# Performance work log

Hardware: AMD Instinct MI355X
Metric: run time of the kernel (lower is better)

The kernel has to match this reference:

```python
import jax, jax.numpy as jnp
import numpy as np

EPS = 1e-5  # InstanceNorm2d default eps


def setup_inputs() -> dict:
    key = jax.random.key(0)
    k1, k2, k3, k4, k5, k6 = jax.random.split(key, 6)
    B, N, C, KV, H = 8, 4096, 512, 960, 4
    dq, dk = C // 4, KV // 4
    emb1 = jax.random.normal(k1, (B, N, C), dtype=jnp.float32)
    emb_all = jax.random.normal(k2, (B, N, KV), dtype=jnp.float32)
    # per-head query Linear weights (torch Linear weight is [out, in]); 4 distinct heads
    Wq = jax.random.normal(k3, (H, dq, dq), dtype=jnp.float32) * 0.05
    # key/value: the original forward only ever uses key[0] / value[0]
    Wk = jax.random.normal(k4, (dk, dk), dtype=jnp.float32) * 0.05
    Wv = jax.random.normal(k5, (dk, dk), dtype=jnp.float32) * 0.05
    Wo = jax.random.normal(k6, (C, C), dtype=jnp.float32) * 0.05
    return {"emb1": emb1, "emb_all": emb_all, "Wq": Wq, "Wk": Wk, "Wv": Wv, "Wo": Wo}


def reference(emb1, emb_all, Wq, Wk, Wv, Wo):
    B, N, C = emb1.shape
    KV = emb_all.shape[2]
    dq, dk = C // 4, KV // 4
    # split emb1 into 4 chunks along channels -> [B, N, 4, dq], apply per-head query Linear
    Qc = emb1.reshape(B, N, 4, dq)
    Q = jnp.einsum("bnhd,hed->bhne", Qc, Wq)            # [B,4,N,dq]
    # all 4 K and V chunks use key[0]/value[0] (as in the source)
    Kc = emb_all.reshape(B, N, 4, dk)
    K = jnp.einsum("bnhd,ed->bhne", Kc, Wk)             # [B,4,N,dk]
    V = jnp.einsum("bnhd,ed->bhne", Kc, Wv)             # [B,4,N,dk]
    # channel attention: contract over tokens N -> scores [B,4,dq,dk]
    scores = jnp.einsum("bhnc,bhnk->bhck", Q, K) / jnp.sqrt(jnp.float32(KV))
    # InstanceNorm2d (no affine): normalize each (b, head) score map over (dq, dk)
    mu = scores.mean(axis=(2, 3), keepdims=True)
    var = scores.var(axis=(2, 3), keepdims=True)        # biased variance, matches torch
    normed = (scores - mu) * jax.lax.rsqrt(var + EPS)
    probs = jax.nn.softmax(normed, axis=3)              # softmax over dk
    # dropout is identity in eval mode
    context = jnp.einsum("bhck,bhnk->bhcn", probs, V)   # [B,4,dq,N]
    # permute(0,3,2,1) -> [B,N,dq,4], flatten last two -> [B,N,C]
    context = jnp.transpose(context, (0, 3, 2, 1)).reshape(B, N, C)
    O1 = jnp.einsum("bnc,ec->bne", context, Wo)         # out Linear, no bias
    return O1
```

## Files before the change

kernel.cpp:

```cpp
#include <hip/hip_runtime.h>
#include <cstdint>
#include <cstddef>

#define B_ 8
#define N_ 4096
#define C_ 512
#define KV_ 960
#define DQ 128
#define DK 240
#define NSPLIT 8

typedef __attribute__((ext_vector_type(8))) short bf16x8;
typedef __attribute__((ext_vector_type(4))) float f32x4;
typedef __attribute__((ext_vector_type(2))) unsigned int u32x2;
#define AS1 __attribute__((address_space(1)))
#define AS3 __attribute__((address_space(3)))

__device__ __forceinline__ ushort f2bf(float f) {
  uint32_t u = __float_as_uint(f);
  u += 0x7FFFu + ((u >> 16) & 1u);
  return (ushort)(u >> 16);
}

union frag_u {
  u32x2 p[2];
  bf16x8 v;
};

#define S_(x) #x
#define SX(x) S_(x)
#define TR8(dst, base, imm) \
  asm volatile("ds_read_b64_tr_b16 %0, %1 offset:" SX(imm) : "=v"(dst) : "v"(base))
#define LDFRAG(dst, base, i1, i2) \
  { frag_u f_; TR8(f_.p[0], base, i1); TR8(f_.p[1], base, i2); dst = f_.v; }

__global__ __launch_bounds__(256) void k_cvt(const float4* __restrict__ in,
                                             ushort4* __restrict__ out, int n4) {
  int i = blockIdx.x * 256 + threadIdx.x;
  if (i >= n4) return;
  float4 v = in[i];
  ushort4 o;
  o.x = f2bf(v.x); o.y = f2bf(v.y); o.z = f2bf(v.z); o.w = f2bf(v.w);
  out[i] = o;
}

__global__ __launch_bounds__(512) void k1_mfma(const ushort* __restrict__ emb1BF,
                                               const ushort* __restrict__ embaBF,
                                               float* __restrict__ P) {
  __shared__ ushort LDS_[2][24576];
  const int bh = blockIdx.x;
  const int split = blockIdx.y;
  const int b = bh >> 2, h = bh & 3;
  const int t = threadIdx.x;
  const int w = t >> 6, l = t & 63;
  const int wr = w >> 2, wn = w & 3;
  const int n0 = split * (N_ / NSPLIT);

  const ushort* srcA[2];
#pragma unroll
  for (int q = 0; q < 2; ++q) {
    uint byte = w * 2048 + q * 1024 + (l << 4);
    uint s = byte >> 7, inner = byte & 127;
    uint jr = inner >> 5, i0 = (inner & 31) >> 1;
    uint g = s & 3, par = (s >> 2) & 1, fmv = (s >> 3) & 7, kv = s >> 6;
    uint noff = kv * 32 + g * 8 + par * 4 + jr;
    srcA[q] = emb1BF + (size_t)b * (N_ * C_) + (size_t)(n0 + noff) * C_ +
              h * DQ + fmv * 16 + i0;
  }
  const ushort* srcB[4];
#pragma unroll
  for (int q = 0; q < 4; ++q) {
    uint byte = w * 4096 + q * 1024 + (l << 4);
    uint s = byte >> 7, inner = byte & 127;
    uint jr = inner >> 5, i0 = (inner & 31) >> 1;
    uint g = s & 3, par = (s >> 2) & 1, jbv = (s >> 3) & 15, kv = s >> 7;
    uint noff = kv * 32 + g * 8 + par * 4 + jr;
    srcB[q] = embaBF + (size_t)b * (N_ * KV_) + (size_t)(n0 + noff) * KV_ +
              h * DK + jbv * 16 + i0;
  }

#define STAGE(tile, bf)                                                        \
  do {                                                                         \
    const size_t nadv = (size_t)(tile) * 64;                                   \
    _Pragma("unroll") for (int q = 0; q < 2; ++q)                              \
        __builtin_amdgcn_global_load_lds(                                      \
            (AS1 const uint32_t*)(uintptr_t)(srcA[q] + nadv * C_),             \
            (AS3 uint32_t*)(uintptr_t)&LDS_[bf][w * 1024 + q * 512], 16, 0, 0);\
    _Pragma("unroll") for (int q = 0; q < 4; ++q)                              \
        __builtin_amdgcn_global_load_lds(                                      \
            (AS1 const uint32_t*)(uintptr_t)(srcB[q] + nadv * KV_),            \
            (AS3 uint32_t*)(uintptr_t)&LDS_[bf][8192 + w * 2048 + q * 512],    \
            16, 0, 0);                                                         \
  } while (0)

  f32x4 acc[4][4];
#pragma unroll
  for (int fm = 0; fm < 4; ++fm)
#pragma unroll
    for (int fn = 0; fn < 4; ++fn) acc[fm][fn] = (f32x4){0.f, 0.f, 0.f, 0.f};

  const uint ldsbase = (uint)(size_t)&LDS_[0][0];
  const uint laneoff = (uint)(l << 3);

#define MMALL()                                                                \
  asm volatile("s_waitcnt lgkmcnt(0)" ::: "memory");                           \
  __builtin_amdgcn_sched_barrier(0);                                           \
  _Pragma("unroll") for (int fm = 0; fm < 4; ++fm)                             \
      _Pragma("unroll") for (int fn = 0; fn < 4; ++fn)                         \
      acc[fm][fn] = __builtin_amdgcn_mfma_f32_16x16x32_bf16(                   \
          af[fm], bv[fn], acc[fm][fn], 0, 0, 0)

  STAGE(0, 0);
  asm volatile("s_waitcnt vmcnt(0)" ::: "memory");
  __builtin_amdgcn_s_barrier();

  for (int ks = 0; ks < 8; ++ks) {
    const int buf = ks & 1;
    if (ks + 1 < 8) STAGE(ks + 1, buf ^ 1);
    const uint aA = ldsbase + (uint)buf * 49152 + (uint)wr * 4096 + laneoff;
    const uint aB = ldsbase + (uint)buf * 49152 + 16384 + (uint)wn * 4096 + laneoff;
    {
      bf16x8 af[4], bv[4];
      LDFRAG(af[0], aA, 0, 512);
      LDFRAG(af[1], aA, 1024, 1536);
      LDFRAG(af[2], aA, 2048, 2560);
      LDFRAG(af[3], aA, 3072, 3584);
      LDFRAG(bv[0], aB, 0, 512);
      LDFRAG(bv[1], aB, 1024, 1536);
      LDFRAG(bv[2], aB, 2048, 2560);
      LDFRAG(bv[3], aB, 3072, 3584);
      MMALL();
    }
    {
      bf16x8 af[4], bv[4];
      LDFRAG(af[0], aA, 8192, 8704);
      LDFRAG(af[1], aA, 9216, 9728);
      LDFRAG(af[2], aA, 10240, 10752);
      LDFRAG(af[3], aA, 11264, 11776);
      LDFRAG(bv[0], aB, 16384, 16896);
      LDFRAG(bv[1], aB, 17408, 17920);
      LDFRAG(bv[2], aB, 18432, 18944);
      LDFRAG(bv[3], aB, 19456, 19968);
      MMALL();
    }
    asm volatile("s_waitcnt vmcnt(0)" ::: "memory");
    __builtin_amdgcn_s_barrier();
  }
#undef STAGE
#undef MMALL

  f32x4* Pv4 = (f32x4*)P + (size_t)(split * 32 + bh) * 8192;
#pragma unroll
  for (int fm = 0; fm < 4; ++fm)
#pragma unroll
    for (int fn = 0; fn < 4; ++fn) Pv4[(fm * 4 + fn) * 512 + t] = acc[fm][fn];
}

__global__ __launch_bounds__(256) void k_reduce_frag(const f32x4* __restrict__ P,
                                                     float* __restrict__ S) {
  const int bh = blockIdx.x;
  const int g = blockIdx.y * 256 + threadIdx.x;
  f32x4 a = P[(size_t)bh * 8192 + g];
#pragma unroll
  for (int s = 1; s < NSPLIT; ++s) {
    f32x4 v = P[(size_t)s * 262144 + (size_t)bh * 8192 + g];
    a.x += v.x; a.y += v.y; a.z += v.z; a.w += v.w;
  }
  const int v = g >> 9, tt = g & 511;
  const int fm = v >> 2, fn = v & 3;
  const int wv = tt >> 6, l = tt & 63;
  const int wr = wv >> 2, wc = wv & 3;
  const int i0 = wr * 64 + fm * 16 + (l >> 4) * 4;
  const int j = wc * 64 + fn * 16 + (l & 15);
  if (j < DK) {
    float* sp = S + (size_t)bh * (DQ * DK) + (size_t)i0 * DK + j;
    sp[0] = a.x; sp[DK] = a.y; sp[2 * DK] = a.z; sp[3 * DK] = a.w;
  }
}

__global__ __launch_bounds__(256) void k_g1(const float* __restrict__ Wq,
                                            const float* __restrict__ S,
                                            float* __restrict__ U) {
  const int h = blockIdx.x, c0 = blockIdx.y * 64;
  const int b = blockIdx.z / 5, n0 = (blockIdx.z % 5) * 48;
  const float* A = Wq + (size_t)h * 16384;
  const float* Bp = S + (size_t)(b * 4 + h) * 30720 + n0;
  float* Cp = U + (size_t)(b * 4 + h) * 30720 + n0;
  __shared__ float Ast[16][65];
  __shared__ float Bst[16][49];
  const int t = threadIdx.x;
  const int mi = (t >> 4) * 4, nj = (t & 15) * 3;
  float acc[4][3] = {};
  for (int k0 = 0; k0 < 128; k0 += 16) {
    __syncthreads();
#pragma unroll
    for (int q = 0; q < 4; ++q) {
      int idx = t + q * 256, m = idx >> 4, k = idx & 15;
      Ast[k][m] = A[(size_t)(c0 + m) * 128 + k0 + k];
    }
#pragma unroll
    for (int q = 0; q < 3; ++q) {
      int idx = t + q * 256, k = idx / 48, n = idx % 48;
      Bst[k][n] = Bp[(size_t)(k0 + k) * 240 + n];
    }
    __syncthreads();
#pragma unroll
    for (int kk = 0; kk < 16; ++kk) {
      float a4[4], b3[3];
#pragma unroll
      for (int x = 0; x < 4; ++x) a4[x] = Ast[kk][mi + x];
#pragma unroll
      for (int y = 0; y < 3; ++y) b3[y] = Bst[kk][nj + y];
#pragma unroll
      for (int x = 0; x < 4; ++x)
#pragma unroll
        for (int y = 0; y < 3; ++y) acc[x][y] = fmaf(a4[x], b3[y], acc[x][y]);
    }
  }
#pragma unroll
  for (int x = 0; x < 4; ++x)
#pragma unroll
    for (int y = 0; y < 3; ++y)
      Cp[(size_t)(c0 + mi + x) * 240 + nj + y] = acc[x][y];
}

__global__ __launch_bounds__(256) void k_g2(const float* __restrict__ U,
                                            const float* __restrict__ Wk,
                                            float* __restrict__ SC) {
  const int m0 = blockIdx.x * 64, n0 = blockIdx.y * 48;
  __shared__ float Ast[16][65];
  __shared__ float Bst2[48][17];
  const int t = threadIdx.x;
  const int mi = (t >> 4) * 4, nj = (t & 15) * 3;
  float acc[4][3] = {};
  for (int k0 = 0; k0 < 240; k0 += 16) {
    __syncthreads();
#pragma unroll
    for (int q = 0; q < 4; ++q) {
      int idx = t + q * 256, m = idx >> 4, k = idx & 15;
      Ast[k][m] = U[(size_t)(m0 + m) * 240 + k0 + k];
    }
#pragma unroll
    for (int q = 0; q < 3; ++q) {
      int idx = t + q * 256, n = idx >> 4, kd = idx & 15;
      Bst2[n][kd] = Wk[(size_t)(n0 + n) * 240 + k0 + kd];
    }
    __syncthreads();
#pragma unroll
    for (int kk = 0; kk < 16; ++kk) {
      float a4[4], b3[3];
#pragma unroll
      for (int x = 0; x < 4; ++x) a4[x] = Ast[kk][mi + x];
#pragma unroll
      for (int y = 0; y < 3; ++y) b3[y] = Bst2[nj + y][kk];
#pragma unroll
      for (int x = 0; x < 4; ++x)
#pragma unroll
        for (int y = 0; y < 3; ++y) acc[x][y] = fmaf(a4[x], b3[y], acc[x][y]);
    }
  }
  const float scale = 0.0322748612183951f;
#pragma unroll
  for (int x = 0; x < 4; ++x)
#pragma unroll
    for (int y = 0; y < 3; ++y)
      SC[(size_t)(m0 + mi + x) * 240 + n0 + nj + y] = acc[x][y] * scale;
}

__global__ __launch_bounds__(256) void k_g3(const float* __restrict__ PR,
                                            const float* __restrict__ Wv,
                                            float* __restrict__ T) {
  const int m0 = blockIdx.x * 64, n0 = blockIdx.y * 48;
  __shared__ float Ast[16][65];
  __shared__ float Bst[16][49];
  const int t = threadIdx.x;
  const int mi = (t >> 4) * 4, nj = (t & 15) * 3;
  float acc[4][3] = {};
  for (int k0 = 0; k0 < 240; k0 += 16) {
    __syncthreads();
#pragma unroll
    for (int q = 0; q < 4; ++q) {
      int idx = t + q * 256, m = idx >> 4, k = idx & 15;
      Ast[k][m] = PR[(size_t)(m0 + m) * 240 + k0 + k];
    }
#pragma unroll
    for (int q = 0; q < 3; ++q) {
      int idx = t + q * 256, k = idx / 48, n = idx % 48;
      Bst[k][n] = Wv[(size_t)(k0 + k) * 240 + n0 + n];
    }
    __syncthreads();
#pragma unroll
    for (int kk = 0; kk < 16; ++kk) {
      float a4[4], b3[3];
#pragma unroll
      for (int x = 0; x < 4; ++x) a4[x] = Ast[kk][mi + x];
#pragma unroll
      for (int y = 0; y < 3; ++y) b3[y] = Bst[kk][nj + y];
#pragma unroll
      for (int x = 0; x < 4; ++x)
#pragma unroll
        for (int y = 0; y < 3; ++y) acc[x][y] = fmaf(a4[x], b3[y], acc[x][y]);
    }
  }
#pragma unroll
  for (int x = 0; x < 4; ++x)
#pragma unroll
    for (int y = 0; y < 3; ++y)
      T[(size_t)(m0 + mi + x) * 240 + n0 + nj + y] = acc[x][y];
}

__global__ __launch_bounds__(256) void k_g4(const float* __restrict__ Wo,
                                            const float* __restrict__ T,
                                            ushort* __restrict__ W3bf) {
  const int h = blockIdx.x, e0 = blockIdx.y * 64;
  const int b = blockIdx.z / 5, n0 = (blockIdx.z % 5) * 48;
  const float* Bp = T + (size_t)(b * 4 + h) * 30720 + n0;
  ushort* Cp = W3bf + (size_t)b * 491520 + h * 240 + n0;
  __shared__ float Ast[16][65];
  __shared__ float Bst[16][49];
  const int t = threadIdx.x;
  const int mi = (t >> 4) * 4, nj = (t & 15) * 3;
  float acc[4][3] = {};
  for (int k0 = 0; k0 < 128; k0 += 16) {
    __syncthreads();
#pragma unroll
    for (int q = 0; q < 4; ++q) {
      int idx = t + q * 256, m = idx >> 4, k = idx & 15;
      Ast[k][m] = Wo[(size_t)(e0 + m) * 512 + 4 * (k0 + k) + h];
    }
#pragma unroll
    for (int q = 0; q < 3; ++q) {
      int idx = t + q * 256, k = idx / 48, n = idx % 48;
      Bst[k][n] = Bp[(size_t)(k0 + k) * 240 + n];
    }
    __syncthreads();
#pragma unroll
    for (int kk = 0; kk < 16; ++kk) {
      float a4[4], b3[3];
#pragma unroll
      for (int x = 0; x < 4; ++x) a4[x] = Ast[kk][mi + x];
#pragma unroll
      for (int y = 0; y < 3; ++y) b3[y] = Bst[kk][nj + y];
#pragma unroll
      for (int x = 0; x < 4; ++x)
#pragma unroll
        for (int y = 0; y < 3; ++y) acc[x][y] = fmaf(a4[x], b3[y], acc[x][y]);
    }
  }
#pragma unroll
  for (int x = 0; x < 4; ++x)
#pragma unroll
    for (int y = 0; y < 3; ++y)
      Cp[(size_t)(e0 + mi + x) * 960 + nj + y] = f2bf(acc[x][y]);
}

__global__ __launch_bounds__(1024) void k_stats(const float* __restrict__ SC,
                                                float* __restrict__ stats) {
  const int bh = blockIdx.x;
  const float* s = SC + (size_t)bh * 30720;
  const int t = threadIdx.x;
  float sum = 0.f, sq = 0.f;
  for (int i = t; i < 30720; i += 1024) {
    float v = s[i];
    sum += v;
    sq = fmaf(v, v, sq);
  }
#pragma unroll
  for (int o = 32; o > 0; o >>= 1) {
    sum += __shfl_down(sum, o);
    sq += __shfl_down(sq, o);
  }
  __shared__ float s1[16], s2[16];
  if ((t & 63) == 0) { s1[t >> 6] = sum; s2[t >> 6] = sq; }
  __syncthreads();
  if (t == 0) {
    float ts = 0.f, tq = 0.f;
#pragma unroll
    for (int i = 0; i < 16; ++i) { ts += s1[i]; tq += s2[i]; }
    const float mu = ts * (1.f / 30720.f);
    const float var = tq * (1.f / 30720.f) - mu * mu;
    stats[bh * 2] = mu;
    stats[bh * 2 + 1] = rsqrtf(var + 1e-5f);
  }
}

__global__ __launch_bounds__(512) void k_softmax(const float* __restrict__ SC,
                                                 const float* __restrict__ stats,
                                                 float* __restrict__ PR) {
  const int bh = blockIdx.x;
  const float mu = stats[bh * 2], rstd = stats[bh * 2 + 1];
  const int wv = threadIdx.x >> 6, l = threadIdx.x & 63;
  const int row0 = blockIdx.y * 32 + wv * 4;
  const float* s = SC + (size_t)bh * 30720;
  float* p = PR + (size_t)bh * 30720;
#pragma unroll
  for (int r = 0; r < 4; ++r) {
    const float* srow = s + (size_t)(row0 + r) * 240;
    float* prow = p + (size_t)(row0 + r) * 240;
    float x0 = (srow[l] - mu) * rstd;
    float x1 = (srow[64 + l] - mu) * rstd;
    float x2 = (srow[128 + l] - mu) * rstd;
    float x3 = (l < 48) ? (srow[192 + l] - mu) * rstd : -1e30f;
    float m = fmaxf(fmaxf(x0, x1), fmaxf(x2, x3));
#pragma unroll
    for (int o = 32; o > 0; o >>= 1) m = fmaxf(m, __shfl_xor(m, o));
    float e0 = __expf(x0 - m), e1 = __expf(x1 - m), e2 = __expf(x2 - m);
    float e3 = (l < 48) ? __expf(x3 - m) : 0.f;
    float ss = e0 + e1 + e2 + e3;
#pragma unroll
    for (int o = 32; o > 0; o >>= 1) ss += __shfl_xor(ss, o);
    const float inv = 1.f / ss;
    prow[l] = e0 * inv;
    prow[64 + l] = e1 * inv;
    prow[128 + l] = e2 * inv;
    if (l < 48) prow[192 + l] = e3 * inv;
  }
}

__global__ __launch_bounds__(256) void k3_mfma(const ushort* __restrict__ A,
                                               const ushort* __restrict__ Bw,
                                               float* __restrict__ C) {
  __shared__ ushort As[128 * 32];
  __shared__ ushort Bs[128 * 32];
  const int bid = blockIdx.x;
  const int swz = (bid & 7) * 128 + (bid >> 3);
  const int b = swz >> 7;
  const int rem = swz & 127;
  const int mt = rem >> 2, nt = rem & 3;
  const int t = threadIdx.x;
  const int w = t >> 6, l = t & 63;
  const int wr = w >> 1, wc = w & 1;

  const ushort* Ab = A + (size_t)b * N_ * KV_ + (size_t)mt * 128 * KV_;
  const ushort* Bb = Bw + (size_t)b * C_ * KV_ + (size_t)nt * 128 * KV_;

  const int r_l = l >> 2;
  const int c_l = (l & 3) * 8;

  f32x4 acc[4][4];
#pragma unroll
  for (int fm = 0; fm < 4; ++fm)
#pragma unroll
    for (int fn = 0; fn < 4; ++fn) acc[fm][fn] = (f32x4){0.f, 0.f, 0.f, 0.f};

  const int lrow = l & 15;
  const int lk = (l >> 4) * 8;

  for (int k0 = 0; k0 < KV_; k0 += 32) {
#pragma unroll
    for (int inst = 0; inst < 2; ++inst) {
      const int gi = w * 2 + inst;
      const ushort* ga = Ab + (size_t)(gi * 16 + r_l) * KV_ + k0 + c_l;
      __builtin_amdgcn_global_load_lds((AS1 const uint32_t*)(uintptr_t)ga,
                                       (AS3 uint32_t*)(uintptr_t)(As + gi * 512),
                                       16, 0, 0);
      const ushort* gb = Bb + (size_t)(gi * 16 + r_l) * KV_ + k0 + c_l;
      __builtin_amdgcn_global_load_lds((AS1 const uint32_t*)(uintptr_t)gb,
                                       (AS3 uint32_t*)(uintptr_t)(Bs + gi * 512),
                                       16, 0, 0);
    }
    __syncthreads();
    bf16x8 af[4], bfr[4];
#pragma unroll
    for (int fm = 0; fm < 4; ++fm)
      af[fm] = *(const bf16x8*)(As + (wr * 64 + fm * 16 + lrow) * 32 + lk);
#pragma unroll
    for (int fn = 0; fn < 4; ++fn)
      bfr[fn] = *(const bf16x8*)(Bs + (wc * 64 + fn * 16 + lrow) * 32 + lk);
#pragma unroll
    for (int fm = 0; fm < 4; ++fm)
#pragma unroll
      for (int fn = 0; fn < 4; ++fn)
        acc[fm][fn] = __builtin_amdgcn_mfma_f32_16x16x32_bf16(af[fm], bfr[fn],
                                                              acc[fm][fn], 0, 0, 0);
    __syncthreads();
  }

  float* Cb = C + (size_t)b * N_ * C_ + ((size_t)mt * 128) * C_ + nt * 128;
  const int col = wc * 64 + (l & 15);
  const int rbase = wr * 64 + (l >> 4) * 4;
#pragma unroll
  for (int fm = 0; fm < 4; ++fm)
#pragma unroll
    for (int fn = 0; fn < 4; ++fn)
#pragma unroll
      for (int r = 0; r < 4; ++r)
        Cb[(size_t)(rbase + fm * 16 + r) * C_ + col + fn * 16] = acc[fm][fn][r];
}

extern "C" void kernel_launch(void* const* d_in, const int* in_sizes, int n_in,
                              void* d_out, int out_size, void* d_ws, size_t ws_size,
                              hipStream_t stream) {
  const float* emb1 = (const float*)d_in[0];
  const float* emba = (const float*)d_in[1];
  const float* Wq   = (const float*)d_in[2];
  const float* Wk   = (const float*)d_in[3];
  const float* Wv   = (const float*)d_in[4];
  const float* Wo   = (const float*)d_in[5];
  float* out = (float*)d_out;
  char* ws = (char*)d_ws;

  ushort* embaBF = (ushort*)(ws);
  float*  S      = (float*)(ws + 62914560);
  float*  T      = (float*)(ws + 62914560);
  float*  U      = (float*)(ws + 66846720);
  ushort* W3bf   = (ushort*)(ws + 66846720);
  float*  SCb    = (float*)(ws + 70778880);
  float*  PRb    = (float*)(ws + 74711040);
  float*  P      = out;
  ushort* emb1BF = (ushort*)((char*)d_out + 33554432);
  float*  stats  = (float*)(ws + 66846720);

  k_cvt<<<16384, 256, 0, stream>>>((const float4*)emb1, (ushort4*)emb1BF, 4194304);
  k_cvt<<<30720, 256, 0, stream>>>((const float4*)emba, (ushort4*)embaBF, 7864320);

  k1_mfma<<<dim3(32, NSPLIT), 512, 0, stream>>>(emb1BF, embaBF, P);
  k_reduce_frag<<<dim3(32, 32), 256, 0, stream>>>((const f32x4*)P, S);

  k_g1<<<dim3(4, 2, 40), 256, 0, stream>>>(Wq, S, U);
  k_g2<<<dim3(64, 5), 256, 0, stream>>>(U, Wk, SCb);
  k_stats<<<32, 1024, 0, stream>>>(SCb, stats);
  k_softmax<<<dim3(32, 4), 512, 0, stream>>>(SCb, stats, PRb);
  k_g3<<<dim3(64, 5), 256, 0, stream>>>(PRb, Wv, T);
  k_g4<<<dim3(4, 8, 40), 256, 0, stream>>>(Wo, T, W3bf);

  k3_mfma<<<1024, 256, 0, stream>>>(embaBF, W3bf, out);
}
```

Baseline: 249.2 us.

## Pre-transpose inputs to token-major bf16 and use plain LDS reads in first GEMM

Adds a transpose-and-convert kernel that writes emb1 and emb_all as bf16 with tokens contiguous, so the N-contracted GEMM loads K-contiguous rows with an XOR swizzle and uses ordinary vector LDS reads instead of transposing ds_read_b64_tr_b16 loads. The main loop now uses 32-token steps with partial vmcnt waits. The cost is that emb_all is converted twice: once transposed for the first GEMM and again in row-major form for the final GEMM. This adds extra memory traffic for the benefit of a simpler first GEMM.

```diff
diff --git a/kernel.cpp b/kernel.cpp
--- a/kernel.cpp
+++ b/kernel.cpp
@@ -12,7 +12,6 @@
 
 typedef __attribute__((ext_vector_type(8))) short bf16x8;
 typedef __attribute__((ext_vector_type(4))) float f32x4;
-typedef __attribute__((ext_vector_type(2))) unsigned int u32x2;
 #define AS1 __attribute__((address_space(1)))
 #define AS3 __attribute__((address_space(3)))
 
@@ -22,17 +21,31 @@
   return (ushort)(u >> 16);
 }
 
-union frag_u {
-  u32x2 p[2];
-  bf16x8 v;
-};
-
-#define S_(x) #x
-#define SX(x) S_(x)
-#define TR8(dst, base, imm) \
-  asm volatile("ds_read_b64_tr_b16 %0, %1 offset:" SX(imm) : "=v"(dst) : "v"(base))
-#define LDFRAG(dst, base, i1, i2) \
-  { frag_u f_; TR8(f_.p[0], base, i1); TR8(f_.p[1], base, i2); dst = f_.v; }
+__global__ __launch_bounds__(256) void k_tr(const float* __restrict__ in,
+                                            ushort* __restrict__ out, int CH) {
+  __shared__ ushort st[64][80];
+  const int n0 = blockIdx.x * 64;
+  const int c0 = blockIdx.y * 64;
+  const int b = blockIdx.z;
+  const int t = threadIdx.x;
+  const int nr = t >> 2, cg = t & 3;
+  const float* src = in + ((size_t)b * N_ + n0 + nr) * CH + c0 + cg * 16;
+  float4 v[4];
+#pragma unroll
+  for (int q = 0; q < 4; ++q) v[q] = *(const float4*)(src + q * 4);
+#pragma unroll
+  for (int q = 0; q < 4; ++q) {
+    st[cg * 16 + q * 4 + 0][nr] = f2bf(v[q].x);
+    st[cg * 16 + q * 4 + 1][nr] = f2bf(v[q].y);
+    st[cg * 16 + q * 4 + 2][nr] = f2bf(v[q].z);
+    st[cg * 16 + q * 4 + 3][nr] = f2bf(v[q].w);
+  }
+  __syncthreads();
+  const int cr = t >> 2, ng = t & 3;
+  ushort* dst = out + ((size_t)b * CH + c0 + cr) * N_ + n0 + ng * 16;
+  *(bf16x8*)(dst) = *(const bf16x8*)(&st[cr][ng * 16]);
+  *(bf16x8*)(dst + 8) = *(const bf16x8*)(&st[cr][ng * 16 + 8]);
+}
 
 __global__ __launch_bounds__(256) void k_cvt(const float4* __restrict__ in,
                                              ushort4* __restrict__ out, int n4) {
@@ -44,53 +57,46 @@
   out[i] = o;
 }
 
-__global__ __launch_bounds__(512) void k1_mfma(const ushort* __restrict__ emb1BF,
-                                               const ushort* __restrict__ embaBF,
-                                               float* __restrict__ P) {
-  __shared__ ushort LDS_[2][24576];
+__global__ __launch_bounds__(512) void k1_nt(const ushort* __restrict__ emb1T,
+                                             const ushort* __restrict__ embaT,
+                                             float* __restrict__ P) {
+  __shared__ ushort LDS_[2 * 12288];
   const int bh = blockIdx.x;
   const int split = blockIdx.y;
   const int b = bh >> 2, h = bh & 3;
   const int t = threadIdx.x;
   const int w = t >> 6, l = t & 63;
-  const int wr = w >> 2, wn = w & 3;
+  const int wr = w >> 2, wc = w & 3;
   const int n0 = split * (N_ / NSPLIT);
 
-  const ushort* srcA[2];
-#pragma unroll
-  for (int q = 0; q < 2; ++q) {
-    uint byte = w * 2048 + q * 1024 + (l << 4);
-    uint s = byte >> 7, inner = byte & 127;
-    uint jr = inner >> 5, i0 = (inner & 31) >> 1;
-    uint g = s & 3, par = (s >> 2) & 1, fmv = (s >> 3) & 7, kv = s >> 6;
-    uint noff = kv * 32 + g * 8 + par * 4 + jr;
-    srcA[q] = emb1BF + (size_t)b * (N_ * C_) + (size_t)(n0 + noff) * C_ +
-              h * DQ + fmv * 16 + i0;
-  }
-  const ushort* srcB[4];
-#pragma unroll
-  for (int q = 0; q < 4; ++q) {
-    uint byte = w * 4096 + q * 1024 + (l << 4);
-    uint s = byte >> 7, inner = byte & 127;
-    uint jr = inner >> 5, i0 = (inner & 31) >> 1;
-    uint g = s & 3, par = (s >> 2) & 1, jbv = (s >> 3) & 15, kv = s >> 7;
-    uint noff = kv * 32 + g * 8 + par * 4 + jr;
-    srcB[q] = embaBF + (size_t)b * (N_ * KV_) + (size_t)(n0 + noff) * KV_ +
-              h * DK + jbv * 16 + i0;
-  }
-
-#define STAGE(tile, bf)                                                        \
-  do {                                                                         \
-    const size_t nadv = (size_t)(tile) * 64;                                   \
-    _Pragma("unroll") for (int q = 0; q < 2; ++q)                              \
-        __builtin_amdgcn_global_load_lds(                                      \
-            (AS1 const uint32_t*)(uintptr_t)(srcA[q] + nadv * C_),             \
-            (AS3 uint32_t*)(uintptr_t)&LDS_[bf][w * 1024 + q * 512], 16, 0, 0);\
-    _Pragma("unroll") for (int q = 0; q < 4; ++q)                              \
-        __builtin_amdgcn_global_load_lds(                                      \
-            (AS1 const uint32_t*)(uintptr_t)(srcB[q] + nadv * KV_),            \
-            (AS3 uint32_t*)(uintptr_t)&LDS_[bf][8192 + w * 2048 + q * 512],    \
-            16, 0, 0);                                                         \
+  const int d = l >> 2, cp = l & 3;
+  const int rA = w * 16 + d;
+  const int cA = cp ^ ((rA >> 1) & 3);
+  const ushort* srcA = emb1T + ((size_t)(b * 512 + h * 128 + rA) << 12) + n0 + cA * 8;
+  const int jB0 = (w * 2 + 0) * 16 + d;
+  const int jB1 = (w * 2 + 1) * 16 + d;
+  const int cB0 = cp ^ ((jB0 >> 1) & 3);
+  const int cB1 = cp ^ ((jB1 >> 1) & 3);
+  const ushort* srcB0 =
+      embaT + ((size_t)(b * 960 + h * 240 + (jB0 < 240 ? jB0 : 239)) << 12) + n0 + cB0 * 8;
+  const ushort* srcB1 =
+      embaT + ((size_t)(b * 960 + h * 240 + (jB1 < 240 ? jB1 : 239)) << 12) + n0 + cB1 * 8;
+  const uint dA = (uint)(w * 1024 + l * 16);
+  const uint dB0 = (uint)(8192 + (w * 2 + 0) * 1024 + l * 16);
+  const uint dB1 = (uint)(8192 + (w * 2 + 1) * 1024 + l * 16);
+  char* LDSb = (char*)LDS_;
+
+#define STAGE(tile, bf)                                                         \
+  do {                                                                          \
+    __builtin_amdgcn_global_load_lds(                                           \
+        (AS1 const uint32_t*)(uintptr_t)(srcA + (size_t)(tile) * 32),           \
+        (AS3 uint32_t*)(uintptr_t)(LDSb + (bf) * 24576 + dA), 16, 0, 0);        \
+    __builtin_amdgcn_global_load_lds(                                           \
+        (AS1 const uint32_t*)(uintptr_t)(srcB0 + (size_t)(tile) * 32),          \
+        (AS3 uint32_t*)(uintptr_t)(LDSb + (bf) * 24576 + dB0), 16, 0, 0);       \
+    __builtin_amdgcn_global_load_lds(                                           \
+        (AS1 const uint32_t*)(uintptr_t)(srcB1 + (size_t)(tile) * 32),          \
+        (AS3 uint32_t*)(uintptr_t)(LDSb + (bf) * 24576 + dB1), 16, 0, 0);       \
   } while (0)
 
   f32x4 acc[4][4];
@@ -99,55 +105,40 @@
 #pragma unroll
     for (int fn = 0; fn < 4; ++fn) acc[fm][fn] = (f32x4){0.f, 0.f, 0.f, 0.f};
 
-  const uint ldsbase = (uint)(size_t)&LDS_[0][0];
-  const uint laneoff = (uint)(l << 3);
-
-#define MMALL()                                                                \
-  asm volatile("s_waitcnt lgkmcnt(0)" ::: "memory");                           \
-  __builtin_amdgcn_sched_barrier(0);                                           \
-  _Pragma("unroll") for (int fm = 0; fm < 4; ++fm)                             \
-      _Pragma("unroll") for (int fn = 0; fn < 4; ++fn)                         \
-      acc[fm][fn] = __builtin_amdgcn_mfma_f32_16x16x32_bf16(                   \
-          af[fm], bv[fn], acc[fm][fn], 0, 0, 0)
+  const int xk = (l >> 4) ^ ((l >> 1) & 3);
+  int offA[4], offB[4];
+#pragma unroll
+  for (int f = 0; f < 4; ++f) {
+    offA[f] = (wr * 64 + f * 16 + (l & 15)) * 32 + xk * 8;
+    offB[f] = 4096 + (wc * 64 + f * 16 + (l & 15)) * 32 + xk * 8;
+  }
 
   STAGE(0, 0);
-  asm volatile("s_waitcnt vmcnt(0)" ::: "memory");
-  __builtin_amdgcn_s_barrier();
-
-  for (int ks = 0; ks < 8; ++ks) {
+  for (int ks = 0; ks < 16; ++ks) {
     const int buf = ks & 1;
-    if (ks + 1 < 8) STAGE(ks + 1, buf ^ 1);
-    const uint aA = ldsbase + (uint)buf * 49152 + (uint)wr * 4096 + laneoff;
-    const uint aB = ldsbase + (uint)buf * 49152 + 16384 + (uint)wn * 4096 + laneoff;
-    {
-      bf16x8 af[4], bv[4];
-      LDFRAG(af[0], aA, 0, 512);
-      LDFRAG(af[1], aA, 1024, 1536);
-      LDFRAG(af[2], aA, 2048, 2560);
-      LDFRAG(af[3], aA, 3072, 3584);
-      LDFRAG(bv[0], aB, 0, 512);
-      LDFRAG(bv[1], aB, 1024, 1536);
-      LDFRAG(bv[2], aB, 2048, 2560);
-      LDFRAG(bv[3], aB, 3072, 3584);
-      MMALL();
-    }
-    {
-      bf16x8 af[4], bv[4];
-      LDFRAG(af[0], aA, 8192, 8704);
-      LDFRAG(af[1], aA, 9216, 9728);
-      LDFRAG(af[2], aA, 10240, 10752);
-      LDFRAG(af[3], aA, 11264, 11776);
-      LDFRAG(bv[0], aB, 16384, 16896);
-      LDFRAG(bv[1], aB, 17408, 17920);
-      LDFRAG(bv[2], aB, 18432, 18944);
-      LDFRAG(bv[3], aB, 19456, 19968);
-      MMALL();
-    }
-    asm volatile("s_waitcnt vmcnt(0)" ::: "memory");
+    if (ks < 15) {
+      STAGE(ks + 1, buf ^ 1);
+      asm volatile("s_waitcnt vmcnt(3)" ::: "memory");
+    } else {
+      asm volatile("s_waitcnt vmcnt(0)" ::: "memory");
+    }
+    __builtin_amdgcn_sched_barrier(0);
     __builtin_amdgcn_s_barrier();
+    const int bb = buf * 12288;
+    bf16x8 af[4], bv[4];
+#pragma unroll
+    for (int f = 0; f < 4; ++f) af[f] = *(const bf16x8*)(LDS_ + bb + offA[f]);
+#pragma unroll
+    for (int f = 0; f < 4; ++f) bv[f] = *(const bf16x8*)(LDS_ + bb + offB[f]);
+#pragma unroll
+    for (int fm = 0; fm < 4; ++fm)
+#pragma unroll
+      for (int fn = 0; fn < 4; ++fn)
+        acc[fm][fn] = __builtin_amdgcn_mfma_f32_16x16x32_bf16(af[fm], bv[fn],
+                                                              acc[fm][fn], 0, 0, 0);
+    __builtin_amdgcn_s_barrier();
   }
 #undef STAGE
-#undef MMALL
 
   f32x4* Pv4 = (f32x4*)P + (size_t)(split * 32 + bh) * 8192;
 #pragma unroll
@@ -500,6 +491,7 @@
   float* out = (float*)d_out;
   char* ws = (char*)d_ws;
 
+  ushort* embaT  = (ushort*)(ws);
   ushort* embaBF = (ushort*)(ws);
   float*  S      = (float*)(ws + 62914560);
   float*  T      = (float*)(ws + 62914560);
@@ -508,14 +500,16 @@
   float*  SCb    = (float*)(ws + 70778880);
   float*  PRb    = (float*)(ws + 74711040);
   float*  P      = out;
-  ushort* emb1BF = (ushort*)((char*)d_out + 33554432);
+  ushort* emb1T  = (ushort*)((char*)d_out + 33554432);
   float*  stats  = (float*)(ws + 66846720);
 
-  k_cvt<<<16384, 256, 0, stream>>>((const float4*)emb1, (ushort4*)emb1BF, 4194304);
+  k_tr<<<dim3(64, 8, 8), 256, 0, stream>>>(emb1, emb1T, 512);
+  k_tr<<<dim3(64, 15, 8), 256, 0, stream>>>(emba, embaT, 960);
+
+  k1_nt<<<dim3(32, NSPLIT), 512, 0, stream>>>(emb1T, embaT, P);
+  k_reduce_frag<<<dim3(32, 32), 256, 0, stream>>>((const f32x4*)P, S);
+
   k_cvt<<<30720, 256, 0, stream>>>((const float4*)emba, (ushort4*)embaBF, 7864320);
-
-  k1_mfma<<<dim3(32, NSPLIT), 512, 0, stream>>>(emb1BF, embaBF, P);
-  k_reduce_frag<<<dim3(32, 32), 256, 0, stream>>>((const f32x4*)P, S);
 
   k_g1<<<dim3(4, 2, 40), 256, 0, stream>>>(Wq, S, U);
   k_g2<<<dim3(64, 5), 256, 0, stream>>>(U, Wk, SCb);
```

Measured after the change: 273.9 us. 9.9% more time.
